# Kernel optimization log

Hardware: AMD Instinct MI355X
Metric: run time of the kernel (lower is better)

## Reference

```python
import jax, jax.numpy as jnp
import numpy as np

N = 100000
E = 1600000
F_DIM = 128
H_DIM = 64
K_CLUSTERS = 16
NEG_SLOPE = 0.2


def setup_inputs() -> dict:
    key = jax.random.key(0)
    ks = jax.random.split(key, 10)
    X = jax.random.normal(ks[0], (N, F_DIM), dtype=jnp.float32)
    ei_feat = jax.random.randint(ks[1], (2, E), 0, N, dtype=jnp.int64)
    batch = jnp.zeros((N,), dtype=jnp.int64)
    # GATv2Conv layer 1 params (heads=1): lin_l, lin_r [F,H], att [H], bias [H]
    s1 = 1.0 / np.sqrt(F_DIM)
    W1l = jax.random.uniform(ks[2], (F_DIM, H_DIM), jnp.float32, -s1, s1)
    W1r = jax.random.uniform(ks[3], (F_DIM, H_DIM), jnp.float32, -s1, s1)
    a1 = jax.random.uniform(ks[4], (H_DIM,), jnp.float32, -1/np.sqrt(H_DIM), 1/np.sqrt(H_DIM))
    b1 = jnp.zeros((H_DIM,), jnp.float32)
    # layer 2: [H,K]
    s2 = 1.0 / np.sqrt(H_DIM)
    W2l = jax.random.uniform(ks[5], (H_DIM, K_CLUSTERS), jnp.float32, -s2, s2)
    W2r = jax.random.uniform(ks[6], (H_DIM, K_CLUSTERS), jnp.float32, -s2, s2)
    a2 = jax.random.uniform(ks[7], (K_CLUSTERS,), jnp.float32, -1/np.sqrt(K_CLUSTERS), 1/np.sqrt(K_CLUSTERS))
    b2 = jnp.zeros((K_CLUSTERS,), jnp.float32)
    return {"X": X, "ei_feat": ei_feat, "batch": batch,
            "W1l": W1l, "W1r": W1r, "a1": a1, "b1": b1,
            "W2l": W2l, "W2r": W2r, "a2": a2, "b2": b2}


def gatv2_conv(x, src, dst, Wl, Wr, a, b, n_nodes):
    # GATv2 (heads=1): e_ij = a^T LeakyReLU(Wl x_j + Wr x_i); softmax over j->i; out_i = sum alpha * Wl x_j
    xl = x @ Wl            # [N,H] source transform
    xr = x @ Wr            # [N,H] target transform
    e = jax.nn.leaky_relu(xl[src] + xr[dst], NEG_SLOPE) @ a   # [E']
    m = jax.ops.segment_max(e, dst, num_segments=n_nodes)      # stable softmax per target
    w = jnp.exp(e - m[dst])
    denom = jax.ops.segment_sum(w, dst, num_segments=n_nodes)
    alpha = w / denom[dst]  # every node has a self-loop, so denom > 0
    out = jax.ops.segment_sum(alpha[:, None] * xl[src], dst, num_segments=n_nodes)
    return out + b


def reference(X, ei_feat, batch, W1l, W1r, a1, b1, W2l, W2r, a2, b2):
    loop = jnp.arange(N, dtype=ei_feat.dtype)
    src = jnp.concatenate([ei_feat[0], loop])  # add_self_loops=True (PyG default)
    dst = jnp.concatenate([ei_feat[1], loop])
    h = jax.nn.elu(gatv2_conv(X, src, dst, W1l, W1r, a1, b1, N))
    z = gatv2_conv(h, src, dst, W2l, W2r, a2, b2, N)
    return jax.nn.softmax(z, axis=1)
```

## Files before the change

kernel.cpp:

```cpp
#include <hip/hip_runtime.h>
#include <stdint.h>

#define F_DIM 128
#define H_DIM 64
#define K_DIM 16
#define BUK_SH 8
#define NCH 256

typedef _Float16 half2v __attribute__((ext_vector_type(2)));
typedef _Float16 half4 __attribute__((ext_vector_type(4)));
typedef _Float16 f16x8 __attribute__((ext_vector_type(8)));
typedef float f32x4 __attribute__((ext_vector_type(4)));

__global__ __launch_bounds__(256) void k_hist(const int* __restrict__ dst,
                                              int* __restrict__ hist,
                                              int E, int CH, int NBUK) {
    __shared__ int h[512];
    int t = threadIdx.x, c = blockIdx.x;
    for (int i = t; i < NBUK; i += 256) h[i] = 0;
    __syncthreads();
    int s = c * CH, e = min(s + CH, E);
    for (int i = s + t; i < e; i += 256) atomicAdd(&h[dst[i] >> BUK_SH], 1);
    __syncthreads();
    for (int i = t; i < NBUK; i += 256) hist[i * NCH + c] = h[i];
}

__global__ __launch_bounds__(256) void k_scanBkt(int* __restrict__ hist,
                                                 int* __restrict__ bktTot) {
    __shared__ int sh[256];
    int b = blockIdx.x, t = threadIdx.x;
    int v = hist[b * NCH + t];
    sh[t] = v;
    __syncthreads();
    for (int off = 1; off < 256; off <<= 1) {
        int x = (t >= off) ? sh[t - off] : 0;
        __syncthreads();
        sh[t] += x;
        __syncthreads();
    }
    hist[b * NCH + t] = sh[t] - v;
    if (t == 255) bktTot[b] = sh[255];
}

__global__ __launch_bounds__(256) void k_scanTot(const int* __restrict__ bktTot,
                                                 int* __restrict__ bktBase, int NBUK) {
    __shared__ int sh[256];
    int t = threadIdx.x;
    int i0 = 2 * t, i1 = 2 * t + 1;
    int v0 = (i0 < NBUK) ? bktTot[i0] : 0;
    int v1 = (i1 < NBUK) ? bktTot[i1] : 0;
    int s = v0 + v1;
    sh[t] = s;
    __syncthreads();
    for (int off = 1; off < 256; off <<= 1) {
        int x = (t >= off) ? sh[t - off] : 0;
        __syncthreads();
        sh[t] += x;
        __syncthreads();
    }
    int excl = sh[t] - s;
    if (i0 < NBUK) bktBase[i0] = excl;
    if (i1 < NBUK) bktBase[i1] = excl + v0;
    if (t == 255) bktBase[NBUK] = sh[255];
}

__global__ __launch_bounds__(256) void k_scatter(const int* __restrict__ src,
                                                 const int* __restrict__ dst,
                                                 const int* __restrict__ hist,
                                                 const int* __restrict__ bktBase,
                                                 uint32_t* __restrict__ binned,
                                                 int E, int CH, int NBUK) {
    __shared__ int ctr[512];
    int t = threadIdx.x, c = blockIdx.x;
    for (int i = t; i < NBUK; i += 256) ctr[i] = bktBase[i] + hist[i * NCH + c];
    __syncthreads();
    int s = c * CH, e = min(s + CH, E);
    for (int i = s + t; i < e; i += 256) {
        int d = dst[i];
        int pos = atomicAdd(&ctr[d >> BUK_SH], 1);
        binned[pos] = (uint32_t)src[i] | ((uint32_t)(d & 255) << 20);
    }
}

__global__ __launch_bounds__(256) void k_fine2(const uint32_t* __restrict__ binned,
                                               const int* __restrict__ bktBase,
                                               int* __restrict__ rowptr,
                                               int* __restrict__ col, int N) {
    __shared__ int h[256], sc[256], slotL[256];
    int b = blockIdx.x, t = threadIdx.x;
    int n0 = b << BUK_SH;
    int s = bktBase[b], e = bktBase[b + 1];
    h[t] = 0;
    __syncthreads();
    for (int i = s + t; i < e; i += 256) atomicAdd(&h[binned[i] >> 20], 1);
    __syncthreads();
    int v = h[t];
    sc[t] = v;
    __syncthreads();
    for (int off = 1; off < 256; off <<= 1) {
        int x = (t >= off) ? sc[t - off] : 0;
        __syncthreads();
        sc[t] += x;
        __syncthreads();
    }
    int excl = sc[t] - v;
    int n = n0 + t;
    int rowbase = s + n0;
    if (n < N) {
        int rp = rowbase + excl + t;
        rowptr[n] = rp;
        col[rp] = n;
        slotL[t] = rp + 1;
        if (n == N - 1) rowptr[N] = rp + v + 1;
    }
    __syncthreads();
    for (int i = s + t; i < e; i += 256) {
        uint32_t p = binned[i];
        int pos = atomicAdd(&slotL[p >> 20], 1);
        col[pos] = (int)(p & 0xFFFFFu);
    }
}

__global__ __launch_bounds__(256) void k_swzW(const float* __restrict__ W1l,
                                              const float* __restrict__ W1r,
                                              const float* __restrict__ W2l,
                                              const float* __restrict__ W2r,
                                              _Float16* __restrict__ Wg1,
                                              _Float16* __restrict__ Wg2) {
    int t = threadIdx.x;
    if (blockIdx.x == 0) {
        for (int i = t; i < 4096; i += 256) {
            int k = i >> 5, c4 = (i & 31) << 2;
            float4 v = (c4 < 64) ? *(const float4*)&W1l[k * 64 + c4]
                                 : *(const float4*)&W1r[k * 64 + (c4 - 64)];
            int s = k >> 5, q = (k >> 3) & 3, j = k & 7;
            float vv[4] = {v.x, v.y, v.z, v.w};
#pragma unroll
            for (int u = 0; u < 4; ++u) {
                int C = c4 + u, c = C >> 4, n = C & 15;
                Wg1[(((c * 4 + s) * 4 + q) * 16 + n) * 8 + j] = (_Float16)vv[u];
            }
        }
    } else {
        for (int i = t; i < 512; i += 256) {
            int k = i >> 3, c4 = (i & 7) << 2;
            float4 v = (c4 < 16) ? *(const float4*)&W2l[k * 16 + c4]
                                 : *(const float4*)&W2r[k * 16 + (c4 - 16)];
            int s = k >> 5, q = (k >> 3) & 3, j = k & 7;
            float vv[4] = {v.x, v.y, v.z, v.w};
#pragma unroll
            for (int u = 0; u < 4; ++u) {
                int C = c4 + u, c = C >> 4, n = C & 15;
                Wg2[(((c * 2 + s) * 4 + q) * 16 + n) * 8 + j] = (_Float16)vv[u];
            }
        }
    }
}

__global__ __launch_bounds__(256, 4) void k_gemm1m(
        const float* __restrict__ X, const _Float16* __restrict__ Wg,
        _Float16* __restrict__ xlh, _Float16* __restrict__ xrh, int N) {
    __shared__ _Float16 Ws[16384];
    int t = threadIdx.x;
    int n0 = blockIdx.x * 64;
    int w = t >> 6, lane = t & 63, m = lane & 15, q = lane >> 4;
#pragma unroll
    for (int i = 0; i < 8; ++i)
        *(f16x8*)&Ws[(i * 256 + t) * 8] = *(const f16x8*)&Wg[(i * 256 + t) * 8];
    int r0 = n0 + w * 16 + m;
    bool v0 = r0 < N;
    const float* p0 = X + (long)r0 * 128 + q * 8;
    const float4 z4 = {0.f, 0.f, 0.f, 0.f};
    float4 xf[8];
#pragma unroll
    for (int s = 0; s < 4; ++s) {
        xf[2 * s]     = v0 ? *(const float4*)(p0 + s * 32)     : z4;
        xf[2 * s + 1] = v0 ? *(const float4*)(p0 + s * 32 + 4) : z4;
    }
    f16x8 af[4];
#pragma unroll
    for (int s = 0; s < 4; ++s) {
        af[s][0] = (_Float16)xf[2 * s].x;     af[s][1] = (_Float16)xf[2 * s].y;
        af[s][2] = (_Float16)xf[2 * s].z;     af[s][3] = (_Float16)xf[2 * s].w;
        af[s][4] = (_Float16)xf[2 * s + 1].x; af[s][5] = (_Float16)xf[2 * s + 1].y;
        af[s][6] = (_Float16)xf[2 * s + 1].z; af[s][7] = (_Float16)xf[2 * s + 1].w;
    }
    __syncthreads();
    f32x4 acc[8];
#pragma unroll
    for (int c = 0; c < 8; ++c) acc[c] = (f32x4){0.f, 0.f, 0.f, 0.f};
#pragma unroll
    for (int s = 0; s < 4; ++s)
#pragma unroll
        for (int c = 0; c < 8; ++c) {
            f16x8 b = *(const f16x8*)&Ws[(((c * 4 + s) * 4 + q) * 16 + m) * 8];
            acc[c] = __builtin_amdgcn_mfma_f32_16x16x32_f16(af[s], b, acc[c], 0, 0, 0);
        }
    __syncthreads();
    _Float16* Tw = &Ws[w * 16 * 136];
#pragma unroll
    for (int c = 0; c < 8; ++c)
#pragma unroll
        for (int r = 0; r < 4; ++r)
            Tw[(q * 4 + r) * 136 + c * 16 + m] = (_Float16)acc[c][r];
    int lr = lane >> 2;
    int gn = n0 + w * 16 + lr;
#pragma unroll
    for (int p = 0; p < 4; ++p) {
        int cc = p * 4 + (lane & 3);
        f16x8 v = *(const f16x8*)&Tw[lr * 136 + cc * 8];
        if (gn < N) {
            if (cc < 8) *(f16x8*)&xlh[(long)gn * 64 + cc * 8] = v;
            else        *(f16x8*)&xrh[(long)gn * 64 + (cc - 8) * 8] = v;
        }
    }
}

__global__ __launch_bounds__(256, 4) void k_gemm2m(
        const _Float16* __restrict__ Hm, const _Float16* __restrict__ Wg2,
        _Float16* __restrict__ xlh, _Float16* __restrict__ xrh, int N) {
    __shared__ _Float16 Ws2[1024];
    __shared__ _Float16 T[4][32 * 40];
    int t = threadIdx.x;
    int n0 = blockIdx.x * 128;
    int w = t >> 6, lane = t & 63, m = lane & 15, q = lane >> 4;
    if (t < 128) *(f16x8*)&Ws2[t * 8] = *(const f16x8*)&Wg2[t * 8];
    const f16x8 zh = {0, 0, 0, 0, 0, 0, 0, 0};
    f16x8 a[2][2];
#pragma unroll
    for (int sub = 0; sub < 2; ++sub) {
        int row = n0 + w * 32 + sub * 16 + m;
        bool vr = row < N;
#pragma unroll
        for (int s = 0; s < 2; ++s)
            a[sub][s] = vr ? *(const f16x8*)&Hm[(long)row * 64 + s * 32 + q * 8] : zh;
    }
    __syncthreads();
    f32x4 acc[2][2];
#pragma unroll
    for (int sub = 0; sub < 2; ++sub)
#pragma unroll
        for (int c = 0; c < 2; ++c) acc[sub][c] = (f32x4){0.f, 0.f, 0.f, 0.f};
#pragma unroll
    for (int s = 0; s < 2; ++s)
#pragma unroll
        for (int c = 0; c < 2; ++c) {
            f16x8 b = *(const f16x8*)&Ws2[(((c * 2 + s) * 4 + q) * 16 + m) * 8];
#pragma unroll
            for (int sub = 0; sub < 2; ++sub)
                acc[sub][c] = __builtin_amdgcn_mfma_f32_16x16x32_f16(a[sub][s], b, acc[sub][c], 0, 0, 0);
        }
    _Float16* Tw = T[w];
#pragma unroll
    for (int sub = 0; sub < 2; ++sub)
#pragma unroll
    for (int c = 0; c < 2; ++c)
#pragma unroll
    for (int r = 0; r < 4; ++r)
        Tw[(sub * 16 + q * 4 + r) * 40 + c * 16 + m] = (_Float16)acc[sub][c][r];
    int lr = lane >> 1;
    int gn = n0 + w * 32 + lr;
#pragma unroll
    for (int p = 0; p < 2; ++p) {
        int cc = p * 2 + (lane & 1);
        f16x8 v = *(const f16x8*)&Tw[lr * 40 + cc * 8];
        if (gn < N) {
            if (cc < 2) *(f16x8*)&xlh[(long)gn * 16 + cc * 8] = v;
            else        *(f16x8*)&xrh[(long)gn * 16 + (cc - 2) * 8] = v;
        }
    }
}

__global__ void k_att1(const f16x8* __restrict__ xlh, const f16x8* __restrict__ xrh,
                       const float* __restrict__ a1, const float* __restrict__ b1,
                       const int* __restrict__ rowptr, const int* __restrict__ col,
                       f16x8* __restrict__ hout, int N) {
    int n = (int)((blockIdx.x * (unsigned)blockDim.x + threadIdx.x) >> 4);
    int lane = threadIdx.x & 63;
    if (n >= N) return;
    int q = lane & 7;
    int g = (lane >> 3) & 1;
    float4 af0 = ((const float4*)a1)[q * 2 + 0];
    float4 af1 = ((const float4*)a1)[q * 2 + 1];
    half2v a01 = {(_Float16)af0.x, (_Float16)af0.y};
    half2v a23 = {(_Float16)af0.z, (_Float16)af0.w};
    half2v a45 = {(_Float16)af1.x, (_Float16)af1.y};
    half2v a67 = {(_Float16)af1.z, (_Float16)af1.w};
    f16x8 xrv = xrh[(long)n * 8 + q];
    int jb = rowptr[n], je = rowptr[n + 1];
    float l = 0.f;
    float o[8] = {0.f, 0.f, 0.f, 0.f, 0.f, 0.f, 0.f, 0.f};
    int j = jb + g;
    for (; j + 2 < je; j += 4) {
        int s0 = col[j], s1 = col[j + 2];
        f16x8 xh0 = xlh[(long)s0 * 8 + q];
        f16x8 xh1 = xlh[(long)s1 * 8 + q];
        f16x8 t0 = xh0 + xrv, t1 = xh1 + xrv;
        f16x8 u0 = __builtin_elementwise_max(t0, t0 * (_Float16)0.2f);
        f16x8 u1 = __builtin_elementwise_max(t1, t1 * (_Float16)0.2f);
        half2v u0a = {u0[0], u0[1]}, u0b = {u0[2], u0[3]}, u0c = {u0[4], u0[5]}, u0d = {u0[6], u0[7]};
        half2v u1a = {u1[0], u1[1]}, u1b = {u1[2], u1[3]}, u1c = {u1[4], u1[5]}, u1d = {u1[6], u1[7]};
        float e0 = __builtin_amdgcn_fdot2(u0a, a01,
                    __builtin_amdgcn_fdot2(u0b, a23,
                     __builtin_amdgcn_fdot2(u0c, a45,
                      __builtin_amdgcn_fdot2(u0d, a67, 0.f, false), false), false), false);
        float e1 = __builtin_amdgcn_fdot2(u1a, a01,
                    __builtin_amdgcn_fdot2(u1b, a23,
                     __builtin_amdgcn_fdot2(u1c, a45,
                      __builtin_amdgcn_fdot2(u1d, a67, 0.f, false), false), false), false);
#pragma unroll
        for (int off = 1; off < 8; off <<= 1) {
            e0 += __shfl_xor(e0, off, 8);
            e1 += __shfl_xor(e1, off, 8);
        }
        float c0 = __expf(e0), c1 = __expf(e1);
        l += c0 + c1;
#pragma unroll
        for (int i = 0; i < 8; ++i)
            o[i] = fmaf(c0, (float)xh0[i], fmaf(c1, (float)xh1[i], o[i]));
    }
    for (; j < je; j += 2) {
        int s = col[j];
        f16x8 xh = xlh[(long)s * 8 + q];
        f16x8 t = xh + xrv;
        f16x8 u = __builtin_elementwise_max(t, t * (_Float16)0.2f);
        half2v ua = {u[0], u[1]}, ub = {u[2], u[3]}, uc = {u[4], u[5]}, ud = {u[6], u[7]};
        float e = __builtin_amdgcn_fdot2(ua, a01,
                   __builtin_amdgcn_fdot2(ub, a23,
                    __builtin_amdgcn_fdot2(uc, a45,
                     __builtin_amdgcn_fdot2(ud, a67, 0.f, false), false), false), false);
#pragma unroll
        for (int off = 1; off < 8; off <<= 1) e += __shfl_xor(e, off, 8);
        float c = __expf(e);
        l += c;
#pragma unroll
        for (int i = 0; i < 8; ++i) o[i] = fmaf(c, (float)xh[i], o[i]);
    }
    l += __shfl_xor(l, 8);
#pragma unroll
    for (int i = 0; i < 8; ++i) o[i] += __shfl_xor(o[i], 8);
    if (g == 0) {
        float4 bv0 = ((const float4*)b1)[q * 2 + 0];
        float4 bv1 = ((const float4*)b1)[q * 2 + 1];
        float bb[8] = {bv0.x, bv0.y, bv0.z, bv0.w, bv1.x, bv1.y, bv1.z, bv1.w};
        float rl = 1.f / l;
        f16x8 hv;
#pragma unroll
        for (int i = 0; i < 8; ++i) {
            float h = o[i] * rl + bb[i];
            h = (h > 0.f) ? h : (__expf(h) - 1.f);
            hv[i] = (_Float16)h;
        }
        hout[(long)n * 8 + q] = hv;
    }
}

__global__ void k_att2(const half4* __restrict__ xlh, const half4* __restrict__ xrh,
                       const float* __restrict__ a2, const float* __restrict__ b2v,
                       const int* __restrict__ rowptr, const int* __restrict__ col,
                       float* __restrict__ out, int N) {
    int n = (int)((blockIdx.x * (unsigned)blockDim.x + threadIdx.x) >> 4);
    int lane = threadIdx.x & 63;
    if (n >= N) return;
    int q = lane & 3;
    int g = (lane >> 2) & 3;
    float4 af = ((const float4*)a2)[q];
    half2v alo = {(_Float16)af.x, (_Float16)af.y};
    half2v ahi = {(_Float16)af.z, (_Float16)af.w};
    half4 xrv = xrh[(long)n * 4 + q];
    int jb = rowptr[n], je = rowptr[n + 1];
    float l = 0.f;
    float4 o = {0.f, 0.f, 0.f, 0.f};
    int j = jb + g;
    for (; j + 4 < je; j += 8) {
        int s0 = col[j], s1 = col[j + 4];
        half4 xh0 = xlh[(long)s0 * 4 + q];
        half4 xh1 = xlh[(long)s1 * 4 + q];
        half4 t0 = xh0 + xrv, t1 = xh1 + xrv;
        half4 u0 = __builtin_elementwise_max(t0, t0 * (_Float16)0.2f);
        half4 u1 = __builtin_elementwise_max(t1, t1 * (_Float16)0.2f);
        half2v u0lo = {u0.x, u0.y}, u0hi = {u0.z, u0.w};
        half2v u1lo = {u1.x, u1.y}, u1hi = {u1.z, u1.w};
        float e0 = __builtin_amdgcn_fdot2(u0lo, alo,
                    __builtin_amdgcn_fdot2(u0hi, ahi, 0.f, false), false);
        float e1 = __builtin_amdgcn_fdot2(u1lo, alo,
                    __builtin_amdgcn_fdot2(u1hi, ahi, 0.f, false), false);
        e0 += __shfl_xor(e0, 1, 4); e0 += __shfl_xor(e0, 2, 4);
        e1 += __shfl_xor(e1, 1, 4); e1 += __shfl_xor(e1, 2, 4);
        float c0 = __expf(e0), c1 = __expf(e1);
        l += c0 + c1;
        o.x = fmaf(c0, (float)xh0.x, fmaf(c1, (float)xh1.x, o.x));
        o.y = fmaf(c0, (float)xh0.y, fmaf(c1, (float)xh1.y, o.y));
        o.z = fmaf(c0, (float)xh0.z, fmaf(c1, (float)xh1.z, o.z));
        o.w = fmaf(c0, (float)xh0.w, fmaf(c1, (float)xh1.w, o.w));
    }
    for (; j < je; j += 4) {
        int s = col[j];
        half4 xh = xlh[(long)s * 4 + q];
        half4 t = xh + xrv;
        half4 u = __builtin_elementwise_max(t, t * (_Float16)0.2f);
        half2v ulo = {u.x, u.y}, uhi = {u.z, u.w};
        float e = __builtin_amdgcn_fdot2(ulo, alo,
                   __builtin_amdgcn_fdot2(uhi, ahi, 0.f, false), false);
        e += __shfl_xor(e, 1, 4);
        e += __shfl_xor(e, 2, 4);
        float c = __expf(e);
        l += c;
        o.x = fmaf(c, (float)xh.x, o.x);
        o.y = fmaf(c, (float)xh.y, o.y);
        o.z = fmaf(c, (float)xh.z, o.z);
        o.w = fmaf(c, (float)xh.w, o.w);
    }
#pragma unroll
    for (int off = 4; off <= 8; off <<= 1) {
        l   += __shfl_xor(l, off);
        o.x += __shfl_xor(o.x, off);
        o.y += __shfl_xor(o.y, off);
        o.z += __shfl_xor(o.z, off);
        o.w += __shfl_xor(o.w, off);
    }
    if (g == 0) {
        float4 bv = ((const float4*)b2v)[q];
        float rl = 1.f / l;
        float4 z;
        z.x = o.x * rl + bv.x;
        z.y = o.y * rl + bv.y;
        z.z = o.z * rl + bv.z;
        z.w = o.w * rl + bv.w;
        float mx = fmaxf(fmaxf(z.x, z.y), fmaxf(z.z, z.w));
        mx = fmaxf(mx, __shfl_xor(mx, 1, 4));
        mx = fmaxf(mx, __shfl_xor(mx, 2, 4));
        float4 ez;
        ez.x = __expf(z.x - mx); ez.y = __expf(z.y - mx);
        ez.z = __expf(z.z - mx); ez.w = __expf(z.w - mx);
        float ss = ez.x + ez.y + ez.z + ez.w;
        ss += __shfl_xor(ss, 1, 4);
        ss += __shfl_xor(ss, 2, 4);
        float rs = 1.f / ss;
        ez.x *= rs; ez.y *= rs; ez.z *= rs; ez.w *= rs;
        ((float4*)out)[(long)n * 4 + q] = ez;
    }
}

extern "C" void kernel_launch(void* const* d_in, const int* in_sizes, int n_in,
                              void* d_out, int out_size, void* d_ws, size_t ws_size,
                              hipStream_t stream) {
    const float* X   = (const float*)d_in[0];
    const int*   ei  = (const int*)d_in[1];
    const float* W1l = (const float*)d_in[3];
    const float* W1r = (const float*)d_in[4];
    const float* a1  = (const float*)d_in[5];
    const float* b1  = (const float*)d_in[6];
    const float* W2l = (const float*)d_in[7];
    const float* W2r = (const float*)d_in[8];
    const float* a2  = (const float*)d_in[9];
    const float* b2  = (const float*)d_in[10];

    int N = in_sizes[0] / F_DIM;
    int E = in_sizes[1] / 2;
    int M = E + N;
    int NBUK = (N + 255) >> BUK_SH;
    int NH = NBUK * NCH;
    int CH = (E + NCH - 1) / NCH;
    const int* srcv = ei;
    const int* dstv = ei + E;

    char* w = (char*)d_ws;
    size_t off = 0;
    auto alloc = [&](size_t bytes) -> char* {
        char* p = w + off;
        off = (off + bytes + 255) & ~(size_t)255;
        return p;
    };
    int* rowptr  = (int*)alloc((size_t)(N + 1) * sizeof(int));
    int* hist    = (int*)alloc((size_t)NH * sizeof(int));
    int* bktTot  = (int*)alloc((size_t)NBUK * sizeof(int));
    int* bktBase = (int*)alloc((size_t)(NBUK + 1) * sizeof(int));
    int* col     = (int*)alloc((size_t)M * sizeof(int));
    uint32_t* binned = (uint32_t*)alloc((size_t)E * sizeof(uint32_t));
    _Float16* xl1h = (_Float16*)alloc((size_t)N * H_DIM * 2);
    _Float16* xr1h = (_Float16*)alloc((size_t)N * H_DIM * 2);
    _Float16* h1h  = (_Float16*)alloc((size_t)N * H_DIM * 2);
    _Float16* xl2h = (_Float16*)alloc((size_t)N * K_DIM * 2);
    _Float16* xr2h = (_Float16*)alloc((size_t)N * K_DIM * 2);
    _Float16* Wg1  = (_Float16*)alloc((size_t)16384 * 2);
    _Float16* Wg2  = (_Float16*)alloc((size_t)2048 * 2);

    k_swzW<<<2, 256, 0, stream>>>(W1l, W1r, W2l, W2r, Wg1, Wg2);
    k_hist<<<NCH, 256, 0, stream>>>(dstv, hist, E, CH, NBUK);
    k_scanBkt<<<NBUK, 256, 0, stream>>>(hist, bktTot);
    k_scanTot<<<1, 256, 0, stream>>>(bktTot, bktBase, NBUK);
    k_scatter<<<NCH, 256, 0, stream>>>(srcv, dstv, hist, bktBase, binned, E, CH, NBUK);
    k_fine2<<<NBUK, 256, 0, stream>>>(binned, bktBase, rowptr, col, N);

    int g1Blocks = (N + 63) / 64;
    k_gemm1m<<<g1Blocks, 256, 0, stream>>>(X, Wg1, xl1h, xr1h, N);
    int nodeBlocks16 = (N + 15) / 16;
    k_att1<<<nodeBlocks16, 256, 0, stream>>>((const f16x8*)xl1h, (const f16x8*)xr1h,
                                             a1, b1, rowptr, col, (f16x8*)h1h, N);
    int g2Blocks = (N + 127) / 128;
    k_gemm2m<<<g2Blocks, 256, 0, stream>>>(h1h, Wg2, xl2h, xr2h, N);
    k_att2<<<nodeBlocks16, 256, 0, stream>>>((const half4*)xl2h, (const half4*)xr2h,
                                             a2, b2, rowptr, col, (float*)d_out, N);
}
```

Baseline: 260.7 us.

## Split GEMM1 columns across warps and load weights via global_load_lds

The first-layer GEMM now covers 32 rows per block instead of 64. Two warps share each 16-row slice, one computing the xl columns and the other the xr columns, so each warp issues half the MFMAs and holds half the accumulators. The 32KB weight staging now uses direct global-to-LDS loads rather than going through registers. Out-of-range rows are clamped to N-1 instead of being masked to zero. The trade-off is twice as many blocks, each reloading the full 32KB of weights into LDS and each reading the X rows twice (once per column half), in exchange for shorter per-warp dependency chains and lower register pressure.

```diff
diff --git a/kernel.cpp b/kernel.cpp
--- a/kernel.cpp
+++ b/kernel.cpp
@@ -11,6 +11,12 @@
 typedef _Float16 half4 __attribute__((ext_vector_type(4)));
 typedef _Float16 f16x8 __attribute__((ext_vector_type(8)));
 typedef float f32x4 __attribute__((ext_vector_type(4)));
+
+__device__ __forceinline__ void gload_lds16(const void* g, void* l) {
+    __builtin_amdgcn_global_load_lds(
+        (const __attribute__((address_space(1))) void*)g,
+        (__attribute__((address_space(3))) void*)l, 16, 0, 0);
+}
 
 __global__ __launch_bounds__(256) void k_hist(const int* __restrict__ dst,
                                               int* __restrict__ hist,
@@ -162,20 +168,25 @@
         _Float16* __restrict__ xlh, _Float16* __restrict__ xrh, int N) {
     __shared__ _Float16 Ws[16384];
     int t = threadIdx.x;
-    int n0 = blockIdx.x * 64;
+    int n0 = blockIdx.x * 32;
     int w = t >> 6, lane = t & 63, m = lane & 15, q = lane >> 4;
-#pragma unroll
-    for (int i = 0; i < 8; ++i)
-        *(f16x8*)&Ws[(i * 256 + t) * 8] = *(const f16x8*)&Wg[(i * 256 + t) * 8];
-    int r0 = n0 + w * 16 + m;
-    bool v0 = r0 < N;
-    const float* p0 = X + (long)r0 * 128 + q * 8;
-    const float4 z4 = {0.f, 0.f, 0.f, 0.f};
+    int rowHalf = w >> 1, cHalf = w & 1;
+    {
+        int base = w * 64;
+#pragma unroll
+        for (int i = 0; i < 8; ++i) {
+            int ch = i * 256 + base;
+            gload_lds16(&Wg[(long)(ch + lane) * 8], &Ws[(long)ch * 8]);
+        }
+    }
+    int r0 = n0 + rowHalf * 16 + m;
+    int rc = (r0 < N) ? r0 : (N - 1);
+    const float* p0 = X + (long)rc * 128 + q * 8;
     float4 xf[8];
 #pragma unroll
     for (int s = 0; s < 4; ++s) {
-        xf[2 * s]     = v0 ? *(const float4*)(p0 + s * 32)     : z4;
-        xf[2 * s + 1] = v0 ? *(const float4*)(p0 + s * 32 + 4) : z4;
+        xf[2 * s]     = *(const float4*)(p0 + s * 32);
+        xf[2 * s + 1] = *(const float4*)(p0 + s * 32 + 4);
     }
     f16x8 af[4];
 #pragma unroll
@@ -186,32 +197,33 @@
         af[s][6] = (_Float16)xf[2 * s + 1].z; af[s][7] = (_Float16)xf[2 * s + 1].w;
     }
     __syncthreads();
-    f32x4 acc[8];
-#pragma unroll
-    for (int c = 0; c < 8; ++c) acc[c] = (f32x4){0.f, 0.f, 0.f, 0.f};
+    f32x4 acc[4];
+#pragma unroll
+    for (int c = 0; c < 4; ++c) acc[c] = (f32x4){0.f, 0.f, 0.f, 0.f};
 #pragma unroll
     for (int s = 0; s < 4; ++s)
 #pragma unroll
-        for (int c = 0; c < 8; ++c) {
-            f16x8 b = *(const f16x8*)&Ws[(((c * 4 + s) * 4 + q) * 16 + m) * 8];
+        for (int c = 0; c < 4; ++c) {
+            int cc = cHalf * 4 + c;
+            f16x8 b = *(const f16x8*)&Ws[(((cc * 4 + s) * 4 + q) * 16 + m) * 8];
             acc[c] = __builtin_amdgcn_mfma_f32_16x16x32_f16(af[s], b, acc[c], 0, 0, 0);
         }
     __syncthreads();
-    _Float16* Tw = &Ws[w * 16 * 136];
-#pragma unroll
-    for (int c = 0; c < 8; ++c)
+    _Float16* Tw = &Ws[w * 2048];
+#pragma unroll
+    for (int c = 0; c < 4; ++c)
 #pragma unroll
         for (int r = 0; r < 4; ++r)
-            Tw[(q * 4 + r) * 136 + c * 16 + m] = (_Float16)acc[c][r];
-    int lr = lane >> 2;
-    int gn = n0 + w * 16 + lr;
-#pragma unroll
-    for (int p = 0; p < 4; ++p) {
-        int cc = p * 4 + (lane & 3);
-        f16x8 v = *(const f16x8*)&Tw[lr * 136 + cc * 8];
+            Tw[(q * 4 + r) * 76 + c * 16 + m] = (_Float16)acc[c][r];
+#pragma unroll
+    for (int p = 0; p < 2; ++p) {
+        int lr = p * 8 + (lane >> 3);
+        int chk = lane & 7;
+        f16x8 v = *(const f16x8*)&Tw[lr * 76 + chk * 8];
+        int gn = n0 + rowHalf * 16 + lr;
         if (gn < N) {
-            if (cc < 8) *(f16x8*)&xlh[(long)gn * 64 + cc * 8] = v;
-            else        *(f16x8*)&xrh[(long)gn * 64 + (cc - 8) * 8] = v;
+            if (cHalf == 0) *(f16x8*)&xlh[(long)gn * 64 + chk * 8] = v;
+            else            *(f16x8*)&xrh[(long)gn * 64 + chk * 8] = v;
         }
     }
 }
@@ -493,7 +505,7 @@
     k_scatter<<<NCH, 256, 0, stream>>>(srcv, dstv, hist, bktBase, binned, E, CH, NBUK);
     k_fine2<<<NBUK, 256, 0, stream>>>(binned, bktBase, rowptr, col, N);
 
-    int g1Blocks = (N + 63) / 64;
+    int g1Blocks = (N + 31) / 32;
     k_gemm1m<<<g1Blocks, 256, 0, stream>>>(X, Wg1, xl1h, xr1h, N);
     int nodeBlocks16 = (N + 15) / 16;
     k_att1<<<nodeBlocks16, 256, 0, stream>>>((const f16x8*)xl1h, (const f16x8*)xr1h,
```

Result: faster. 238.4 us (-8.6%).
